# Kernel optimization log

Measured on AMD Instinct MI355X. Metric: run time of the kernel, lower is better.

## Reference

```python
import jax, jax.numpy as jnp
import numpy as np

N = 20000   # nodes
E = 200000  # directed edges (~kNN k=5, bidirectional)
IN = 256    # in_channels
D = 512     # projected_channels = in_channels * 2
NEG_SLOPE = 0.2


def _ln(x, g, b):
    mu = x.mean(-1, keepdims=True)
    var = ((x - mu) ** 2).mean(-1, keepdims=True)
    return (x - mu) * jax.lax.rsqrt(var + 1e-5) * g + b


def _gat(x, src, dst, W, a_s, a_d, bias, concat):
    # PyG GATConv: linear -> per-edge leaky-relu attention -> segment softmax over dst -> scatter-add
    n = x.shape[0]
    H, C = a_s.shape
    h = (x @ W).reshape(n, H, C)                      # [N,H,C]
    as_n = jnp.einsum('nhc,hc->nh', h, a_s)           # alpha contribution of src node
    ad_n = jnp.einsum('nhc,hc->nh', h, a_d)           # alpha contribution of dst node
    e = jax.nn.leaky_relu(as_n[src] + ad_n[dst], negative_slope=NEG_SLOPE)  # [E,H]
    m = jax.ops.segment_max(e, dst, num_segments=n)   # stable softmax per dst (self-loops => every dst nonempty)
    ex = jnp.exp(e - m[dst])
    den = jax.ops.segment_sum(ex, dst, num_segments=n)
    alpha = ex / den[dst]                             # [E,H]
    out = jax.ops.segment_sum(h[src] * alpha[:, :, None], dst, num_segments=n)  # [N,H,C]
    out = out.reshape(n, H * C) if concat else out.mean(axis=1)
    return out + bias


def setup_inputs() -> dict:
    key = jax.random.key(0)
    ks = jax.random.split(key, 40)
    x = jax.random.normal(ks[0], (N, IN), jnp.float32)
    src = jax.random.randint(ks[1], (E,), 0, N)
    off = jax.random.randint(ks[2], (E,), 1, N)
    dst = (src + off) % N                              # guarantees src != dst
    edge_index = jnp.stack([src, dst]).astype(jnp.int64)

    def p(k, shape, fan):
        return (jax.random.normal(k, shape, jnp.float32) / np.float32(np.sqrt(fan)))

    inp = {
        'x': x, 'edge_index': edge_index,
        'proj_W': p(ks[3], (IN, D), IN), 'proj_b': jnp.zeros((D,), jnp.float32),
        'blk_norm_g': jnp.ones((3, D), jnp.float32), 'blk_norm_b': jnp.zeros((3, D), jnp.float32),
        'g1_W': p(ks[4], (3, D, D), D), 'g1_as': p(ks[5], (3, 4, 128), 128), 'g1_ad': p(ks[6], (3, 4, 128), 128),
        'g1_b': jnp.zeros((3, D), jnp.float32),
        'g2_W': p(ks[7], (3, D, 128), D), 'g2_as': p(ks[8], (3, 2, 64), 64), 'g2_ad': p(ks[9], (3, 2, 64), 64),
        'g2_b': jnp.zeros((3, 128), jnp.float32),
        'uni_W': p(ks[10], (3, 640, D), 640), 'uni_b': jnp.zeros((3, D), jnp.float32),
        'fin_g': jnp.ones((D,), jnp.float32), 'fin_b': jnp.zeros((D,), jnp.float32),
        'fg_W': p(ks[11], (D, 8 * 128), D), 'fg_as': p(ks[12], (8, 128), 128), 'fg_ad': p(ks[13], (8, 128), 128),
        'fg_b': jnp.zeros((128,), jnp.float32),
    }
    return inp


def reference(x, edge_index, proj_W, proj_b, blk_norm_g, blk_norm_b,
              g1_W, g1_as, g1_ad, g1_b, g2_W, g2_as, g2_ad, g2_b,
              uni_W, uni_b, fin_g, fin_b, fg_W, fg_as, fg_ad, fg_b):
    n = x.shape[0]
    loops = jnp.arange(n, dtype=edge_index.dtype)
    src = jnp.concatenate([edge_index[0], loops])     # add_self_loops (PyG default)
    dst = jnp.concatenate([edge_index[1], loops])

    x = jax.nn.elu(x @ proj_W + proj_b)
    for i in range(3):
        res = x
        xn = _ln(x, blk_norm_g[i], blk_norm_b[i])
        o1 = _gat(xn, src, dst, g1_W[i], g1_as[i], g1_ad[i], g1_b[i], True)
        o2 = _gat(xn, src, dst, g2_W[i], g2_as[i], g2_ad[i], g2_b[i], True)
        xc = jax.nn.elu(jnp.concatenate([o1, o2], axis=-1))
        x = res + xc @ uni_W[i] + uni_b[i]
        x = jax.nn.elu(x)
    x = _ln(x, fin_g, fin_b)
    return _gat(x, src, dst, fg_W, fg_as, fg_ad, fg_b, False)  # heads=8, concat=False -> mean
```

## Files before the change

### kernel.cpp

```cpp
#include <hip/hip_runtime.h>
#include <math.h>

#define NN 20000
#define EDGES 200000
#define MPAD 20096

using short8  = __attribute__((ext_vector_type(8))) short;
using short4v = __attribute__((ext_vector_type(4))) short;
using f32x4   = __attribute__((ext_vector_type(4))) float;
typedef unsigned short ushortT;
typedef unsigned int uintT;

__device__ __forceinline__ ushortT f2bfu(float x) {
  union { float f; unsigned u; } c; c.f = x;
  unsigned r = c.u + 0x7FFFu + ((c.u >> 16) & 1u);
  return (ushortT)(r >> 16);
}
__device__ __forceinline__ float bflo(uintT u) {
  union { unsigned i; float f; } c; c.i = u << 16; return c.f;
}
__device__ __forceinline__ float bfhi(uintT u) {
  union { unsigned i; float f; } c; c.i = u & 0xFFFF0000u; return c.f;
}
__device__ __forceinline__ float elu_f(float v) { return v > 0.f ? v : (expf(v) - 1.f); }

__device__ __forceinline__ void acc8(float* acc, uint4 u, float a) {
  acc[0] += a * bflo(u.x); acc[1] += a * bfhi(u.x);
  acc[2] += a * bflo(u.y); acc[3] += a * bfhi(u.y);
  acc[4] += a * bflo(u.z); acc[5] += a * bfhi(u.z);
  acc[6] += a * bflo(u.w); acc[7] += a * bfhi(u.w);
}

__global__ void k_hist(const int* __restrict__ ei, int* __restrict__ cnt) {
  int i = blockIdx.x * 256 + threadIdx.x;
  const int EE = EDGES + NN;
  if (i >= EE) return;
  int d = (i < EDGES) ? ei[EDGES + i] : (i - EDGES);
  atomicAdd(&cnt[d], 1);
}

__global__ __launch_bounds__(256) void k_scan1(const int* __restrict__ cnt,
                                               int* __restrict__ bsum, int n) {
  int b = blockIdx.x, t = threadIdx.x, i = b * 256 + t;
  int v = (i < n) ? cnt[i] : 0;
#pragma unroll
  for (int off = 32; off > 0; off >>= 1) v += __shfl_down(v, off);
  __shared__ int s[4];
  if ((t & 63) == 0) s[t >> 6] = v;
  __syncthreads();
  if (t == 0) bsum[b] = s[0] + s[1] + s[2] + s[3];
}

__global__ void k_scan2(const int* __restrict__ bsum, int* __restrict__ boff,
                        int nb, int* __restrict__ ptr, int n) {
  if (threadIdx.x == 0) {
    int acc = 0;
    for (int b = 0; b < nb; ++b) { boff[b] = acc; acc += bsum[b]; }
    ptr[n] = acc;
  }
}

__global__ __launch_bounds__(256) void k_scan3(const int* __restrict__ cnt,
                                               const int* __restrict__ boff,
                                               int* __restrict__ ptr,
                                               int* __restrict__ cursor, int n) {
  __shared__ int sd[256];
  int b = blockIdx.x, t = threadIdx.x, i = b * 256 + t;
  int v = (i < n) ? cnt[i] : 0;
  sd[t] = v;
  __syncthreads();
  for (int off = 1; off < 256; off <<= 1) {
    int a = (t >= off) ? sd[t - off] : 0;
    __syncthreads();
    sd[t] += a;
    __syncthreads();
  }
  if (i < n) {
    int p = boff[b] + sd[t] - v;
    ptr[i] = p;
    cursor[i] = p;
  }
}

__global__ void k_scatter(const int* __restrict__ ei, int* __restrict__ cursor,
                          int* __restrict__ ssrc) {
  int i = blockIdx.x * 256 + threadIdx.x;
  const int EE = EDGES + NN;
  if (i >= EE) return;
  int s, d;
  if (i < EDGES) { s = ei[i]; d = ei[EDGES + i]; }
  else           { s = i - EDGES; d = s; }
  int pos = atomicAdd(&cursor[d], 1);
  ssrc[pos] = s;
}

struct CvtDesc { const float* src; ushortT* dst; int K; int N; int t0; };
struct CvtArgs { CvtDesc d[11]; };

__global__ __launch_bounds__(256) void k_cvtT(CvtArgs a) {
  __shared__ float tile[32][33];
  int b = blockIdx.x;
  int mi = 0;
#pragma unroll
  for (int i = 1; i < 11; ++i)
    if (b >= a.d[i].t0) mi = i;
  CvtDesc dd = a.d[mi];
  int tb = b - dd.t0;
  int tnc = dd.N / 32;
  int tk = tb / tnc, tn = tb % tnc;
  int t = threadIdx.x;
  {
    int r = t >> 3, c4 = (t & 7) * 4;
    float4 v = *reinterpret_cast<const float4*>(&dd.src[(size_t)(tk * 32 + r) * dd.N + tn * 32 + c4]);
    tile[r][c4 + 0] = v.x; tile[r][c4 + 1] = v.y; tile[r][c4 + 2] = v.z; tile[r][c4 + 3] = v.w;
  }
  __syncthreads();
  {
    int n = t >> 3, k4 = (t & 7) * 4;
    short4v s;
    s.x = (short)f2bfu(tile[k4 + 0][n]);
    s.y = (short)f2bfu(tile[k4 + 1][n]);
    s.z = (short)f2bfu(tile[k4 + 2][n]);
    s.w = (short)f2bfu(tile[k4 + 3][n]);
    *reinterpret_cast<short4v*>(&dd.dst[(size_t)(tn * 32 + n) * dd.K + tk * 32 + k4]) = s;
  }
}

__global__ void k_cvtX(const float* __restrict__ in, ushortT* __restrict__ out, int n4) {
  int i = blockIdx.x * 256 + threadIdx.x;
  if (i >= n4) return;
  float4 v = reinterpret_cast<const float4*>(in)[i];
  short4v s;
  s.x = (short)f2bfu(v.x); s.y = (short)f2bfu(v.y);
  s.z = (short)f2bfu(v.z); s.w = (short)f2bfu(v.w);
  reinterpret_cast<short4v*>(out)[i] = s;
}

__global__ __launch_bounds__(256) void k_ln(const float* __restrict__ in,
                                            const float* __restrict__ g,
                                            const float* __restrict__ b,
                                            ushortT* __restrict__ out) {
  int row = blockIdx.x, t = threadIdx.x;
  const float* r = in + (size_t)row * 512;
  float v0 = r[t], v1 = r[t + 256];
  __shared__ float red[4];
  int w = t >> 6, lane = t & 63;
  float s = v0 + v1;
#pragma unroll
  for (int off = 32; off > 0; off >>= 1) s += __shfl_down(s, off);
  if (lane == 0) red[w] = s;
  __syncthreads();
  float mu = (red[0] + red[1] + red[2] + red[3]) * (1.f / 512.f);
  float d0 = v0 - mu, d1 = v1 - mu;
  float vs = d0 * d0 + d1 * d1;
#pragma unroll
  for (int off = 32; off > 0; off >>= 1) vs += __shfl_down(vs, off);
  __syncthreads();
  if (lane == 0) red[w] = vs;
  __syncthreads();
  float var = (red[0] + red[1] + red[2] + red[3]) * (1.f / 512.f);
  float rs = rsqrtf(var + 1e-5f);
  ushortT* o = out + (size_t)row * 512;
  o[t]       = f2bfu(d0 * rs * g[t]       + b[t]);
  o[t + 256] = f2bfu(d1 * rs * g[t + 256] + b[t + 256]);
}

template <int EPI, bool OUTBF16, int NB, int ATT>
__global__ __launch_bounds__(256) void k_gemm(const ushortT* __restrict__ A,
                                              const ushortT* __restrict__ Wt,
                                              const float* __restrict__ bias,
                                              const float* __restrict__ res,
                                              void* __restrict__ Outv,
                                              const float* __restrict__ w1s,
                                              const float* __restrict__ w1d,
                                              const float* __restrict__ w2s,
                                              const float* __restrict__ w2d,
                                              float* __restrict__ as_out,
                                              float* __restrict__ ad_out,
                                              int M, int N, int K) {
  __shared__ short As[128][40];
  __shared__ short Bs[128][40];
  int b = blockIdx.x;
  int x = b & 7, g = b >> 3;
  int mt = x + 8 * (g / NB);
  int nt = g % NB;
  int m0 = mt * 128, n0 = nt * 128;
  if (m0 >= M) return;
  int t = threadIdx.x;
  int w = t >> 6, lane = t & 63;
  int wm = w >> 1, wn = w & 1;
  int lr = lane & 15, lk = (lane >> 4) * 8;
  int sr = t >> 2, sc = (t & 3) * 8;
  int ga0 = m0 + sr, ga1 = m0 + sr + 64;
  const short8 z8 = {};

  short8 vA0, vA1, vB0, vB1;
  {
    vA0 = (ga0 < M) ? *reinterpret_cast<const short8*>(&A[(size_t)ga0 * K + sc]) : z8;
    vA1 = (ga1 < M) ? *reinterpret_cast<const short8*>(&A[(size_t)ga1 * K + sc]) : z8;
    vB0 = *reinterpret_cast<const short8*>(&Wt[(size_t)(n0 + sr) * K + sc]);
    vB1 = *reinterpret_cast<const short8*>(&Wt[(size_t)(n0 + sr + 64) * K + sc]);
  }
  f32x4 acc[4][4] = {};
  for (int k0 = 0; k0 < K; k0 += 32) {
    *reinterpret_cast<short8*>(&As[sr][sc]) = vA0;
    *reinterpret_cast<short8*>(&As[sr + 64][sc]) = vA1;
    *reinterpret_cast<short8*>(&Bs[sr][sc]) = vB0;
    *reinterpret_cast<short8*>(&Bs[sr + 64][sc]) = vB1;
    __syncthreads();
    int k1 = k0 + 32;
    if (k1 < K) {
      vA0 = (ga0 < M) ? *reinterpret_cast<const short8*>(&A[(size_t)ga0 * K + k1 + sc]) : z8;
      vA1 = (ga1 < M) ? *reinterpret_cast<const short8*>(&A[(size_t)ga1 * K + k1 + sc]) : z8;
      vB0 = *reinterpret_cast<const short8*>(&Wt[(size_t)(n0 + sr) * K + k1 + sc]);
      vB1 = *reinterpret_cast<const short8*>(&Wt[(size_t)(n0 + sr + 64) * K + k1 + sc]);
    }
    short8 af[4], bf[4];
#pragma unroll
    for (int m = 0; m < 4; ++m)
      af[m] = *reinterpret_cast<const short8*>(&As[wm * 64 + m * 16 + lr][lk]);
#pragma unroll
    for (int n = 0; n < 4; ++n)
      bf[n] = *reinterpret_cast<const short8*>(&Bs[wn * 64 + n * 16 + lr][lk]);
#pragma unroll
    for (int m = 0; m < 4; ++m)
#pragma unroll
      for (int n = 0; n < 4; ++n)
        acc[m][n] = __builtin_amdgcn_mfma_f32_16x16x32_bf16(af[m], bf[n], acc[m][n], 0, 0, 0);
    __syncthreads();
  }
#pragma unroll
  for (int m = 0; m < 4; ++m) {
#pragma unroll
    for (int n = 0; n < 4; ++n) {
#pragma unroll
      for (int j = 0; j < 4; ++j) {
        int row = wm * 64 + m * 16 + (lane >> 4) * 4 + j;
        int col = wn * 64 + n * 16 + lr;
        int gr = m0 + row, gc = n0 + col;
        if (gr < M) {
          float v = acc[m][n][j];
          if (EPI >= 1) v += bias[gc];
          if (EPI == 2) v += res[(size_t)gr * N + gc];
          if (EPI >= 1) v = elu_f(v);
          if (OUTBF16) ((ushortT*)Outv)[(size_t)gr * N + gc] = f2bfu(v);
          else         ((float*)Outv)[(size_t)gr * N + gc] = v;
        }
      }
    }
  }
  if (ATT) {
    float wsv[4], wdv[4];
#pragma unroll
    for (int n = 0; n < 4; ++n) {
      int gc = n0 + wn * 64 + n * 16 + lr;
      if (ATT == 1) {
        wsv[n] = (gc < 512) ? w1s[gc] : w2s[gc - 512];
        wdv[n] = (gc < 512) ? w1d[gc] : w2d[gc - 512];
      } else {
        wsv[n] = w1s[gc];
        wdv[n] = w1d[gc];
      }
    }
    int hc = n0 + wn * 64;
    int head = (ATT == 1) ? ((hc < 512) ? (hc >> 7) : 4 + ((hc - 512) >> 6))
                          : (hc >> 7);
    const int H = (ATT == 1) ? 6 : 8;
#pragma unroll
    for (int m = 0; m < 4; ++m) {
#pragma unroll
      for (int j = 0; j < 4; ++j) {
        float sa = 0.f, da = 0.f;
#pragma unroll
        for (int n = 0; n < 4; ++n) {
          float v = acc[m][n][j];
          sa += v * wsv[n];
          da += v * wdv[n];
        }
#pragma unroll
        for (int o = 1; o < 16; o <<= 1) {
          sa += __shfl_xor(sa, o, 16);
          da += __shfl_xor(da, o, 16);
        }
        int gr = m0 + wm * 64 + m * 16 + (lane >> 4) * 4 + j;
        if (lr == 0 && gr < M) {
          atomicAdd(&as_out[gr * H + head], sa);
          atomicAdd(&ad_out[gr * H + head], da);
        }
      }
    }
  }
}

__global__ __launch_bounds__(320) void k_agg_blk(const ushortT* __restrict__ h,
                                                 const float* __restrict__ as_n,
                                                 const float* __restrict__ ad_n,
                                                 const int* __restrict__ rowptr,
                                                 const int* __restrict__ ssrc,
                                                 const float* __restrict__ b1,
                                                 const float* __restrict__ b2,
                                                 ushortT* __restrict__ out) {
  int dnode = blockIdx.x;
  int t = threadIdx.x;
  int grp = t / 80;
  int r = t - grp * 80;
  int ch0 = r * 8;
  int head = (ch0 < 512) ? (ch0 >> 7) : (4 + ((ch0 - 512) >> 6));
  int e0 = rowptr[dnode], deg = rowptr[dnode + 1] - e0;
  float acc[8] = {};
  __shared__ float s_alpha[64 * 6];
  __shared__ int s_src[64];
  __shared__ float s_part[4][640];
  __shared__ float s_m[6], s_den[6], s_adv[6];
  if (t < 6) { s_m[t] = -INFINITY; s_den[t] = 0.f; s_adv[t] = ad_n[dnode * 6 + t]; }
  __syncthreads();
  for (int base = 0; base < deg; base += 64) {
    int cnt = min(64, deg - base);
    if (t < cnt) {
      int s = ssrc[e0 + base + t];
      s_src[t] = s;
#pragma unroll
      for (int hh = 0; hh < 6; ++hh) {
        float v = as_n[s * 6 + hh] + s_adv[hh];
        s_alpha[t * 6 + hh] = (v > 0.f) ? v : 0.2f * v;
      }
    }
    __syncthreads();
    if (t < 6) {
      float mx = s_m[t];
      for (int j = 0; j < cnt; ++j) mx = fmaxf(mx, s_alpha[j * 6 + t]);
      float sc = expf(s_m[t] - mx);
      float ds = 0.f;
      for (int j = 0; j < cnt; ++j) ds += expf(s_alpha[j * 6 + t] - mx);
      s_den[t] = s_den[t] * sc + ds;
      s_m[t] = mx;
    }
    __syncthreads();
  }
  if (t < 6) s_den[t] = 1.f / s_den[t];
  __syncthreads();
  for (int base = 0; base < deg; base += 64) {
    int cnt = min(64, deg - base);
    bool regather = (base > 0) || (deg > 64);
    if (regather) {
      __syncthreads();
      if (t < cnt) {
        int s = ssrc[e0 + base + t];
        s_src[t] = s;
#pragma unroll
        for (int hh = 0; hh < 6; ++hh) {
          float v = as_n[s * 6 + hh] + s_adv[hh];
          s_alpha[t * 6 + hh] = (v > 0.f) ? v : 0.2f * v;
        }
      }
      __syncthreads();
    }
    if (t < cnt) {
#pragma unroll
      for (int hh = 0; hh < 6; ++hh)
        s_alpha[t * 6 + hh] = expf(s_alpha[t * 6 + hh] - s_m[hh]) * s_den[hh];
    }
    __syncthreads();
    int jj = grp;
    for (; jj + 4 < cnt; jj += 8) {
      int sA = s_src[jj], sB = s_src[jj + 4];
      uint4 uA = *reinterpret_cast<const uint4*>(h + (size_t)sA * 640 + ch0);
      uint4 uB = *reinterpret_cast<const uint4*>(h + (size_t)sB * 640 + ch0);
      acc8(acc, uA, s_alpha[jj * 6 + head]);
      acc8(acc, uB, s_alpha[(jj + 4) * 6 + head]);
    }
    if (jj < cnt) {
      int sA = s_src[jj];
      uint4 uA = *reinterpret_cast<const uint4*>(h + (size_t)sA * 640 + ch0);
      acc8(acc, uA, s_alpha[jj * 6 + head]);
    }
  }
  __syncthreads();
#pragma unroll
  for (int q = 0; q < 8; ++q) s_part[grp][ch0 + q] = acc[q];
  __syncthreads();
  {
    int ch = t * 2;
    float v0 = s_part[0][ch] + s_part[1][ch] + s_part[2][ch] + s_part[3][ch];
    float v1 = s_part[0][ch + 1] + s_part[1][ch + 1] + s_part[2][ch + 1] + s_part[3][ch + 1];
    v0 += (ch < 512) ? b1[ch] : b2[ch - 512];
    v1 += (ch < 512) ? b1[ch + 1] : b2[ch - 511];
    v0 = elu_f(v0); v1 = elu_f(v1);
    uintT o = (uintT)f2bfu(v0) | ((uintT)f2bfu(v1) << 16);
    *reinterpret_cast<uintT*>(&out[(size_t)dnode * 640 + ch]) = o;
  }
}

__global__ __launch_bounds__(256) void k_agg_mean(
    const ushortT* __restrict__ h, const float* __restrict__ as_n,
    const float* __restrict__ ad_n,
    const int* __restrict__ rowptr, const int* __restrict__ ssrc,
    const float* __restrict__ bias, float* __restrict__ out) {
  int dnode = blockIdx.x;
  int t = threadIdx.x;
  int grp = t >> 7;
  int r = t & 127;
  int head = r >> 4;
  int e0 = rowptr[dnode], deg = rowptr[dnode + 1] - e0;
  float acc[8] = {};
  __shared__ float s_alpha[64 * 8];
  __shared__ int s_src[64];
  __shared__ float s_part[2][1024];
  __shared__ float s_m[8], s_den[8], s_adv[8];
  if (t < 8) { s_m[t] = -INFINITY; s_den[t] = 0.f; s_adv[t] = ad_n[dnode * 8 + t]; }
  __syncthreads();
  for (int base = 0; base < deg; base += 64) {
    int cnt = min(64, deg - base);
    if (t < cnt) {
      int s = ssrc[e0 + base + t];
      s_src[t] = s;
#pragma unroll
      for (int hh = 0; hh < 8; ++hh) {
        float v = as_n[s * 8 + hh] + s_adv[hh];
        s_alpha[t * 8 + hh] = (v > 0.f) ? v : 0.2f * v;
      }
    }
    __syncthreads();
    if (t < 8) {
      float mx = s_m[t];
      for (int j = 0; j < cnt; ++j) mx = fmaxf(mx, s_alpha[j * 8 + t]);
      float sc = expf(s_m[t] - mx);
      float ds = 0.f;
      for (int j = 0; j < cnt; ++j) ds += expf(s_alpha[j * 8 + t] - mx);
      s_den[t] = s_den[t] * sc + ds;
      s_m[t] = mx;
    }
    __syncthreads();
  }
  if (t < 8) s_den[t] = 1.f / s_den[t];
  __syncthreads();
  for (int base = 0; base < deg; base += 64) {
    int cnt = min(64, deg - base);
    bool regather = (base > 0) || (deg > 64);
    if (regather) {
      __syncthreads();
      if (t < cnt) {
        int s = ssrc[e0 + base + t];
        s_src[t] = s;
#pragma unroll
        for (int hh = 0; hh < 8; ++hh) {
          float v = as_n[s * 8 + hh] + s_adv[hh];
          s_alpha[t * 8 + hh] = (v > 0.f) ? v : 0.2f * v;
        }
      }
      __syncthreads();
    }
    if (t < cnt) {
#pragma unroll
      for (int hh = 0; hh < 8; ++hh)
        s_alpha[t * 8 + hh] = expf(s_alpha[t * 8 + hh] - s_m[hh]) * s_den[hh];
    }
    __syncthreads();
    int jj = grp;
    for (; jj + 2 < cnt; jj += 4) {
      int sA = s_src[jj], sB = s_src[jj + 2];
      uint4 uA = *reinterpret_cast<const uint4*>(h + (size_t)sA * 1024 + r * 8);
      uint4 uB = *reinterpret_cast<const uint4*>(h + (size_t)sB * 1024 + r * 8);
      acc8(acc, uA, s_alpha[jj * 8 + head]);
      acc8(acc, uB, s_alpha[(jj + 2) * 8 + head]);
    }
    if (jj < cnt) {
      int sA = s_src[jj];
      uint4 uA = *reinterpret_cast<const uint4*>(h + (size_t)sA * 1024 + r * 8);
      acc8(acc, uA, s_alpha[jj * 8 + head]);
    }
  }
  __syncthreads();
#pragma unroll
  for (int q = 0; q < 8; ++q) s_part[grp][r * 8 + q] = acc[q];
  __syncthreads();
  if (t < 128) {
    float v = 0.f;
#pragma unroll
    for (int hh = 0; hh < 8; ++hh)
      v += s_part[0][hh * 128 + t] + s_part[1][hh * 128 + t];
    out[(size_t)dnode * 128 + t] = v * 0.125f + bias[t];
  }
}

extern "C" void kernel_launch(void* const* d_in, const int* in_sizes, int n_in,
                              void* d_out, int out_size, void* d_ws, size_t ws_size,
                              hipStream_t stream) {
  const float* x_in   = (const float*)d_in[0];
  const int*   ei     = (const int*)d_in[1];
  const float* proj_W = (const float*)d_in[2];
  const float* proj_b = (const float*)d_in[3];
  const float* bng    = (const float*)d_in[4];
  const float* bnb    = (const float*)d_in[5];
  const float* g1W    = (const float*)d_in[6];
  const float* g1as   = (const float*)d_in[7];
  const float* g1ad   = (const float*)d_in[8];
  const float* g1b    = (const float*)d_in[9];
  const float* g2W    = (const float*)d_in[10];
  const float* g2as   = (const float*)d_in[11];
  const float* g2ad   = (const float*)d_in[12];
  const float* g2b    = (const float*)d_in[13];
  const float* uniW   = (const float*)d_in[14];
  const float* unib   = (const float*)d_in[15];
  const float* fing   = (const float*)d_in[16];
  const float* finb   = (const float*)d_in[17];
  const float* fgW    = (const float*)d_in[18];
  const float* fgas   = (const float*)d_in[19];
  const float* fgad   = (const float*)d_in[20];
  const float* fgb    = (const float*)d_in[21];

  const int EE = EDGES + NN;
  char* ws = (char*)d_ws;
  size_t off = 0;
  auto alloc = [&](size_t bytes) -> void* {
    void* p = ws + off;
    off += (bytes + 255) & ~(size_t)255;
    return p;
  };
  float*   xA    = (float*)alloc((size_t)NN * 512 * 4);
  float*   xB    = (float*)alloc((size_t)NN * 512 * 4);
  ushortT* xn    = (ushortT*)alloc((size_t)MPAD * 512 * 2);
  ushortT* xinb  = (ushortT*)alloc((size_t)MPAD * 256 * 2);
  ushortT* hcat  = (ushortT*)alloc((size_t)NN * 640 * 2);
  ushortT* xc    = (ushortT*)alloc((size_t)MPAD * 640 * 2);
  float*   asb   = (float*)alloc((size_t)NN * 8 * 4);
  float*   adb   = (float*)alloc((size_t)NN * 8 * 4);
  ushortT* projT = (ushortT*)alloc((size_t)512 * 256 * 2);
  ushortT* gcatT = (ushortT*)alloc((size_t)3 * 640 * 512 * 2);
  ushortT* uniT  = (ushortT*)alloc((size_t)3 * 512 * 640 * 2);
  ushortT* fgT   = (ushortT*)alloc((size_t)1024 * 512 * 2);
  int* cnt    = (int*)alloc((size_t)NN * 4);
  int* ptr    = (int*)alloc((size_t)(NN + 1) * 4);
  int* cursor = (int*)alloc((size_t)NN * 4);
  int* ssrc   = (int*)alloc((size_t)EE * 4);
  int* bsum   = (int*)alloc((size_t)128 * 4);
  int* boff   = (int*)alloc((size_t)128 * 4);
  ushortT* hf = hcat;

  const int NB79 = (NN + 255) / 256;

  hipMemsetAsync(cnt, 0, (size_t)NN * 4, stream);
  k_hist<<<(EE + 255) / 256, 256, 0, stream>>>(ei, cnt);
  k_scan1<<<NB79, 256, 0, stream>>>(cnt, bsum, NN);
  k_scan2<<<1, 64, 0, stream>>>(bsum, boff, NB79, ptr, NN);
  k_scan3<<<NB79, 256, 0, stream>>>(cnt, boff, ptr, cursor, NN);
  k_scatter<<<(EE + 255) / 256, 256, 0, stream>>>(ei, cursor, ssrc);

  {
    CvtArgs a;
    int t0 = 0;
    auto add = [&](int idx, const float* s, ushortT* d, int K, int N) {
      a.d[idx] = { s, d, K, N, t0 };
      t0 += (K / 32) * (N / 32);
    };
    add(0, proj_W, projT, 256, 512);
    for (int i = 0; i < 3; ++i)
      add(1 + i, g1W + (size_t)i * 512 * 512, gcatT + (size_t)i * 640 * 512, 512, 512);
    for (int i = 0; i < 3; ++i)
      add(4 + i, g2W + (size_t)i * 512 * 128, gcatT + (size_t)i * 640 * 512 + 512 * 512, 512, 128);
    for (int i = 0; i < 3; ++i)
      add(7 + i, uniW + (size_t)i * 640 * 512, uniT + (size_t)i * 512 * 640, 640, 512);
    add(10, fgW, fgT, 512, 1024);
    k_cvtT<<<t0, 256, 0, stream>>>(a);
  }
  k_cvtX<<<(NN * 256 / 4 + 255) / 256, 256, 0, stream>>>(x_in, xinb, NN * 256 / 4);

  const int GMP = 160;

  k_gemm<1, false, 4, 0><<<GMP * 4, 256, 0, stream>>>(
      xinb, projT, proj_b, nullptr, xA,
      nullptr, nullptr, nullptr, nullptr, nullptr, nullptr, NN, 512, 256);

  float* cur = xA;
  float* alt = xB;
  for (int i = 0; i < 3; ++i) {
    k_ln<<<NN, 256, 0, stream>>>(cur, bng + i * 512, bnb + i * 512, xn);
    hipMemsetAsync(asb, 0, (size_t)2 * NN * 8 * 4, stream);
    k_gemm<0, true, 5, 1><<<GMP * 5, 256, 0, stream>>>(
        xn, gcatT + (size_t)i * 640 * 512, nullptr, nullptr, hcat,
        g1as + i * 512, g1ad + i * 512, g2as + i * 128, g2ad + i * 128,
        asb, adb, NN, 640, 512);
    k_agg_blk<<<NN, 320, 0, stream>>>(hcat, asb, adb, ptr, ssrc,
                                      g1b + i * 512, g2b + i * 128, xc);
    k_gemm<2, false, 4, 0><<<GMP * 4, 256, 0, stream>>>(
        xc, uniT + (size_t)i * 512 * 640, unib + i * 512, cur, alt,
        nullptr, nullptr, nullptr, nullptr, nullptr, nullptr, NN, 512, 640);
    float* tmp = cur; cur = alt; alt = tmp;
  }

  k_ln<<<NN, 256, 0, stream>>>(cur, fing, finb, xn);
  hipMemsetAsync(asb, 0, (size_t)2 * NN * 8 * 4, stream);
  k_gemm<0, true, 8, 2><<<GMP * 8, 256, 0, stream>>>(
      xn, fgT, nullptr, nullptr, hf,
      fgas, fgad, nullptr, nullptr, asb, adb, NN, 1024, 512);
  k_agg_mean<<<NN, 256, 0, stream>>>(hf, asb, adb, ptr, ssrc, fgb, (float*)d_out);
}
```

Measured before the change: 836.6 us.

## Replace attention-score atomics with shared reduction; parallelize softmax stats

The GEMM epilogue now reduces per-row attention contributions across the two column warps in shared memory and writes each head score directly. This removes the global atomics and the memsets that cleared the score buffers. The aggregation kernels compute the softmax max and sum with 16 lanes per head using shuffle reductions instead of one serial thread per head. Normalisation by the denominator is deferred to the final per-channel output. It assumes each GEMM column tile covers exactly one head, or the two g2 heads when nt==4, and adds a block barrier in the GEMM epilogue.

```diff
diff --git a/kernel.cpp b/kernel.cpp
--- a/kernel.cpp
+++ b/kernel.cpp
@@ -250,6 +250,8 @@
     }
   }
   if (ATT) {
+    __shared__ float s_as[2][128];
+    __shared__ float s_ad[2][128];
     float wsv[4], wdv[4];
 #pragma unroll
     for (int n = 0; n < 4; ++n) {
@@ -262,10 +264,6 @@
         wdv[n] = w1d[gc];
       }
     }
-    int hc = n0 + wn * 64;
-    int head = (ATT == 1) ? ((hc < 512) ? (hc >> 7) : 4 + ((hc - 512) >> 6))
-                          : (hc >> 7);
-    const int H = (ATT == 1) ? 6 : 8;
 #pragma unroll
     for (int m = 0; m < 4; ++m) {
 #pragma unroll
@@ -282,10 +280,26 @@
           sa += __shfl_xor(sa, o, 16);
           da += __shfl_xor(da, o, 16);
         }
-        int gr = m0 + wm * 64 + m * 16 + (lane >> 4) * 4 + j;
-        if (lr == 0 && gr < M) {
-          atomicAdd(&as_out[gr * H + head], sa);
-          atomicAdd(&ad_out[gr * H + head], da);
+        if (lr == 0) {
+          int row = wm * 64 + m * 16 + (lane >> 4) * 4 + j;
+          s_as[wn][row] = sa;
+          s_ad[wn][row] = da;
+        }
+      }
+    }
+    __syncthreads();
+    if (t < 128) {
+      int gr = m0 + t;
+      if (gr < M) {
+        const int H = (ATT == 1) ? 6 : 8;
+        if (ATT == 1 && nt == 4) {
+          as_out[gr * H + 4] = s_as[0][t];
+          ad_out[gr * H + 4] = s_ad[0][t];
+          as_out[gr * H + 5] = s_as[1][t];
+          ad_out[gr * H + 5] = s_ad[1][t];
+        } else {
+          as_out[gr * H + nt] = s_as[0][t] + s_as[1][t];
+          ad_out[gr * H + nt] = s_ad[0][t] + s_ad[1][t];
         }
       }
     }
@@ -307,13 +321,13 @@
   int ch0 = r * 8;
   int head = (ch0 < 512) ? (ch0 >> 7) : (4 + ((ch0 - 512) >> 6));
   int e0 = rowptr[dnode], deg = rowptr[dnode + 1] - e0;
+  bool multi = deg > 64;
   float acc[8] = {};
-  __shared__ float s_alpha[64 * 6];
+  __shared__ float s_lg[64 * 6];
   __shared__ int s_src[64];
   __shared__ float s_part[4][640];
-  __shared__ float s_m[6], s_den[6], s_adv[6];
-  if (t < 6) { s_m[t] = -INFINITY; s_den[t] = 0.f; s_adv[t] = ad_n[dnode * 6 + t]; }
-  __syncthreads();
+  __shared__ float s_m[6], s_den[6], s_rd[6];
+  if (t < 6) { s_m[t] = -INFINITY; s_den[t] = 0.f; }
   for (int base = 0; base < deg; base += 64) {
     int cnt = min(64, deg - base);
     if (t < cnt) {
@@ -321,36 +335,42 @@
       s_src[t] = s;
 #pragma unroll
       for (int hh = 0; hh < 6; ++hh) {
-        float v = as_n[s * 6 + hh] + s_adv[hh];
-        s_alpha[t * 6 + hh] = (v > 0.f) ? v : 0.2f * v;
-      }
-    }
-    __syncthreads();
-    if (t < 6) {
-      float mx = s_m[t];
-      for (int j = 0; j < cnt; ++j) mx = fmaxf(mx, s_alpha[j * 6 + t]);
-      float sc = expf(s_m[t] - mx);
-      float ds = 0.f;
-      for (int j = 0; j < cnt; ++j) ds += expf(s_alpha[j * 6 + t] - mx);
-      s_den[t] = s_den[t] * sc + ds;
-      s_m[t] = mx;
-    }
-    __syncthreads();
-  }
-  if (t < 6) s_den[t] = 1.f / s_den[t];
-  __syncthreads();
+        float v = as_n[s * 6 + hh] + ad_n[dnode * 6 + hh];
+        s_lg[t * 6 + hh] = (v > 0.f) ? v : 0.2f * v;
+      }
+    }
+    __syncthreads();
+    if (t < 96) {
+      int hh = t >> 4, l = t & 15;
+      float mx = -INFINITY;
+      for (int j = l; j < cnt; j += 16) mx = fmaxf(mx, s_lg[j * 6 + hh]);
+#pragma unroll
+      for (int o = 8; o > 0; o >>= 1) mx = fmaxf(mx, __shfl_xor(mx, o, 16));
+      float sm = 0.f;
+      for (int j = l; j < cnt; j += 16) sm += expf(s_lg[j * 6 + hh] - mx);
+#pragma unroll
+      for (int o = 8; o > 0; o >>= 1) sm += __shfl_xor(sm, o, 16);
+      if (l == 0) {
+        float om = s_m[hh];
+        float nm = fmaxf(om, mx);
+        s_den[hh] = s_den[hh] * expf(om - nm) + sm * expf(mx - nm);
+        s_m[hh] = nm;
+      }
+    }
+    __syncthreads();
+  }
+  if (t < 6) s_rd[t] = 1.f / s_den[t];
   for (int base = 0; base < deg; base += 64) {
     int cnt = min(64, deg - base);
-    bool regather = (base > 0) || (deg > 64);
-    if (regather) {
+    if (multi) {
       __syncthreads();
       if (t < cnt) {
         int s = ssrc[e0 + base + t];
         s_src[t] = s;
 #pragma unroll
         for (int hh = 0; hh < 6; ++hh) {
-          float v = as_n[s * 6 + hh] + s_adv[hh];
-          s_alpha[t * 6 + hh] = (v > 0.f) ? v : 0.2f * v;
+          float v = as_n[s * 6 + hh] + ad_n[dnode * 6 + hh];
+          s_lg[t * 6 + hh] = (v > 0.f) ? v : 0.2f * v;
         }
       }
       __syncthreads();
@@ -358,7 +378,7 @@
     if (t < cnt) {
 #pragma unroll
       for (int hh = 0; hh < 6; ++hh)
-        s_alpha[t * 6 + hh] = expf(s_alpha[t * 6 + hh] - s_m[hh]) * s_den[hh];
+        s_lg[t * 6 + hh] = expf(s_lg[t * 6 + hh] - s_m[hh]);
     }
     __syncthreads();
     int jj = grp;
@@ -366,13 +386,13 @@
       int sA = s_src[jj], sB = s_src[jj + 4];
       uint4 uA = *reinterpret_cast<const uint4*>(h + (size_t)sA * 640 + ch0);
       uint4 uB = *reinterpret_cast<const uint4*>(h + (size_t)sB * 640 + ch0);
-      acc8(acc, uA, s_alpha[jj * 6 + head]);
-      acc8(acc, uB, s_alpha[(jj + 4) * 6 + head]);
+      acc8(acc, uA, s_lg[jj * 6 + head]);
+      acc8(acc, uB, s_lg[(jj + 4) * 6 + head]);
     }
     if (jj < cnt) {
       int sA = s_src[jj];
       uint4 uA = *reinterpret_cast<const uint4*>(h + (size_t)sA * 640 + ch0);
-      acc8(acc, uA, s_alpha[jj * 6 + head]);
+      acc8(acc, uA, s_lg[jj * 6 + head]);
     }
   }
   __syncthreads();
@@ -381,8 +401,11 @@
   __syncthreads();
   {
     int ch = t * 2;
+    int hh = (ch < 512) ? (ch >> 7) : (4 + ((ch - 512) >> 6));
+    float rd = s_rd[hh];
     float v0 = s_part[0][ch] + s_part[1][ch] + s_part[2][ch] + s_part[3][ch];
     float v1 = s_part[0][ch + 1] + s_part[1][ch + 1] + s_part[2][ch + 1] + s_part[3][ch + 1];
+    v0 *= rd; v1 *= rd;
     v0 += (ch < 512) ? b1[ch] : b2[ch - 512];
     v1 += (ch < 512) ? b1[ch + 1] : b2[ch - 511];
     v0 = elu_f(v0); v1 = elu_f(v1);
@@ -402,13 +425,13 @@
   int r = t & 127;
   int head = r >> 4;
   int e0 = rowptr[dnode], deg = rowptr[dnode + 1] - e0;
+  bool multi = deg > 64;
   float acc[8] = {};
-  __shared__ float s_alpha[64 * 8];
+  __shared__ float s_lg[64 * 8];
   __shared__ int s_src[64];
   __shared__ float s_part[2][1024];
-  __shared__ float s_m[8], s_den[8], s_adv[8];
-  if (t < 8) { s_m[t] = -INFINITY; s_den[t] = 0.f; s_adv[t] = ad_n[dnode * 8 + t]; }
-  __syncthreads();
+  __shared__ float s_m[8], s_den[8], s_rd[8];
+  if (t < 8) { s_m[t] = -INFINITY; s_den[t] = 0.f; }
   for (int base = 0; base < deg; base += 64) {
     int cnt = min(64, deg - base);
     if (t < cnt) {
@@ -416,36 +439,42 @@
       s_src[t] = s;
 #pragma unroll
       for (int hh = 0; hh < 8; ++hh) {
-        float v = as_n[s * 8 + hh] + s_adv[hh];
-        s_alpha[t * 8 + hh] = (v > 0.f) ? v : 0.2f * v;
-      }
-    }
-    __syncthreads();
-    if (t < 8) {
-      float mx = s_m[t];
-      for (int j = 0; j < cnt; ++j) mx = fmaxf(mx, s_alpha[j * 8 + t]);
-      float sc = expf(s_m[t] - mx);
-      float ds = 0.f;
-      for (int j = 0; j < cnt; ++j) ds += expf(s_alpha[j * 8 + t] - mx);
-      s_den[t] = s_den[t] * sc + ds;
-      s_m[t] = mx;
-    }
-    __syncthreads();
-  }
-  if (t < 8) s_den[t] = 1.f / s_den[t];
-  __syncthreads();
+        float v = as_n[s * 8 + hh] + ad_n[dnode * 8 + hh];
+        s_lg[t * 8 + hh] = (v > 0.f) ? v : 0.2f * v;
+      }
+    }
+    __syncthreads();
+    if (t < 128) {
+      int hh = t >> 4, l = t & 15;
+      float mx = -INFINITY;
+      for (int j = l; j < cnt; j += 16) mx = fmaxf(mx, s_lg[j * 8 + hh]);
+#pragma unroll
+      for (int o = 8; o > 0; o >>= 1) mx = fmaxf(mx, __shfl_xor(mx, o, 16));
+      float sm = 0.f;
+      for (int j = l; j < cnt; j += 16) sm += expf(s_lg[j * 8 + hh] - mx);
+#pragma unroll
+      for (int o = 8; o > 0; o >>= 1) sm += __shfl_xor(sm, o, 16);
+      if (l == 0) {
+        float om = s_m[hh];
+        float nm = fmaxf(om, mx);
+        s_den[hh] = s_den[hh] * expf(om - nm) + sm * expf(mx - nm);
+        s_m[hh] = nm;
+      }
+    }
+    __syncthreads();
+  }
+  if (t < 8) s_rd[t] = 1.f / s_den[t];
   for (int base = 0; base < deg; base += 64) {
     int cnt = min(64, deg - base);
-    bool regather = (base > 0) || (deg > 64);
-    if (regather) {
+    if (multi) {
       __syncthreads();
       if (t < cnt) {
         int s = ssrc[e0 + base + t];
         s_src[t] = s;
 #pragma unroll
         for (int hh = 0; hh < 8; ++hh) {
-          float v = as_n[s * 8 + hh] + s_adv[hh];
-          s_alpha[t * 8 + hh] = (v > 0.f) ? v : 0.2f * v;
+          float v = as_n[s * 8 + hh] + ad_n[dnode * 8 + hh];
+          s_lg[t * 8 + hh] = (v > 0.f) ? v : 0.2f * v;
         }
       }
       __syncthreads();
@@ -453,7 +482,7 @@
     if (t < cnt) {
 #pragma unroll
       for (int hh = 0; hh < 8; ++hh)
-        s_alpha[t * 8 + hh] = expf(s_alpha[t * 8 + hh] - s_m[hh]) * s_den[hh];
+        s_lg[t * 8 + hh] = expf(s_lg[t * 8 + hh] - s_m[hh]);
     }
     __syncthreads();
     int jj = grp;
@@ -461,13 +490,13 @@
       int sA = s_src[jj], sB = s_src[jj + 2];
       uint4 uA = *reinterpret_cast<const uint4*>(h + (size_t)sA * 1024 + r * 8);
       uint4 uB = *reinterpret_cast<const uint4*>(h + (size_t)sB * 1024 + r * 8);
-      acc8(acc, uA, s_alpha[jj * 8 + head]);
-      acc8(acc, uB, s_alpha[(jj + 2) * 8 + head]);
+      acc8(acc, uA, s_lg[jj * 8 + head]);
+      acc8(acc, uB, s_lg[(jj + 2) * 8 + head]);
     }
     if (jj < cnt) {
       int sA = s_src[jj];
       uint4 uA = *reinterpret_cast<const uint4*>(h + (size_t)sA * 1024 + r * 8);
-      acc8(acc, uA, s_alpha[jj * 8 + head]);
+      acc8(acc, uA, s_lg[jj * 8 + head]);
     }
   }
   __syncthreads();
@@ -477,8 +506,10 @@
   if (t < 128) {
     float v = 0.f;
 #pragma unroll
-    for (int hh = 0; hh < 8; ++hh)
-      v += s_part[0][hh * 128 + t] + s_part[1][hh * 128 + t];
+    for (int hh = 0; hh < 8; ++hh) {
+      float ph = s_part[0][hh * 128 + t] + s_part[1][hh * 128 + t];
+      v += ph * s_rd[hh];
+    }
     out[(size_t)dnode * 128 + t] = v * 0.125f + bias[t];
   }
 }
@@ -575,7 +606,6 @@
   float* alt = xB;
   for (int i = 0; i < 3; ++i) {
     k_ln<<<NN, 256, 0, stream>>>(cur, bng + i * 512, bnb + i * 512, xn);
-    hipMemsetAsync(asb, 0, (size_t)2 * NN * 8 * 4, stream);
     k_gemm<0, true, 5, 1><<<GMP * 5, 256, 0, stream>>>(
         xn, gcatT + (size_t)i * 640 * 512, nullptr, nullptr, hcat,
         g1as + i * 512, g1ad + i * 512, g2as + i * 128, g2ad + i * 128,
@@ -589,7 +619,6 @@
   }
 
   k_ln<<<NN, 256, 0, stream>>>(cur, fing, finb, xn);
-  hipMemsetAsync(asb, 0, (size_t)2 * NN * 8 * 4, stream);
   k_gemm<0, true, 8, 2><<<GMP * 8, 256, 0, stream>>>(
       xn, fgT, nullptr, nullptr, hf,
       fgas, fgad, nullptr, nullptr, asb, adb, NN, 1024, 512);
```

After: 703.8 us. 15.9% less time.
